# Optimization experiments

Measured on AMD Instinct MI355X. Metric: run time of the kernel, lower is better.

## Reference

```python
import jax, jax.numpy as jnp
import numpy as np

D_MODEL = 256
D_INNER = 512   # expand=2
D_STATE = 16
DT_RANK = 16    # ceil(d_model/16)
D_CONV = 4
N_LAYERS = 2    # per direction
B, N = 2, 1024


def _mamba_layer(x, W_in, cw, cb, W_x, W_dt, b_dt, A_log, Dp, W_out):
    """One mamba_ssm.Mamba forward. x: (B, L, d_model)."""
    Bb, L, _ = x.shape
    xz = x @ W_in.T                        # (B, L, 2*d_inner)
    di = xz.shape[-1] // 2
    xc, z = xz[..., :di], xz[..., di:]
    # causal depthwise conv1d, kernel D_CONV, left-pad d_conv-1
    K = cw.shape[-1]
    xp = jnp.pad(xc, ((0, 0), (K - 1, 0), (0, 0)))
    xc = sum(xp[:, k:k + L, :] * cw[:, k] for k in range(K)) + cb
    xc = jax.nn.silu(xc)
    # input-dependent dt, B, C
    dbl = xc @ W_x.T                       # (B, L, dt_rank + 2*d_state)
    ds = A_log.shape[-1]
    dt = dbl[..., :DT_RANK]
    Bm = dbl[..., DT_RANK:DT_RANK + ds]    # (B, L, d_state)
    Cm = dbl[..., DT_RANK + ds:]           # (B, L, d_state)
    dt = jax.nn.softplus(dt @ W_dt.T + b_dt)  # (B, L, d_inner)
    A = -jnp.exp(A_log)                    # (d_inner, d_state)
    dA = jnp.exp(dt[..., None] * A)                          # (B, L, di, ds)
    dBx = dt[..., None] * Bm[:, :, None, :] * xc[..., None]  # (B, L, di, ds)

    def step(h, inp):
        a_t, b_t, c_t = inp                # (B,di,ds),(B,di,ds),(B,ds)
        h = a_t * h + b_t
        y_t = jnp.einsum('bds,bs->bd', h, c_t)
        return h, y_t

    h0 = jnp.zeros((Bb, di, ds), x.dtype)
    _, ys = jax.lax.scan(step, h0, (dA.transpose(1, 0, 2, 3),
                                    dBx.transpose(1, 0, 2, 3),
                                    Cm.transpose(1, 0, 2)))
    y = ys.transpose(1, 0, 2) + xc * Dp    # skip term D*x
    y = y * jax.nn.silu(z)                 # gate
    return y @ W_out.T                     # (B, L, d_model)


def setup_inputs() -> dict:
    key = jax.random.key(0)
    ks = jax.random.split(key, 10)
    s = 0.05  # weight scale for numerical stability
    nlay = 2 * N_LAYERS  # forward layers then backward layers
    return {
        "x": jax.random.normal(ks[0], (B, N, D_MODEL), jnp.float32),
        "in_proj": jax.random.normal(ks[1], (nlay, 2 * D_INNER, D_MODEL), jnp.float32) * s,
        "conv_w": jax.random.normal(ks[2], (nlay, D_INNER, D_CONV), jnp.float32) * s,
        "conv_b": jax.random.normal(ks[3], (nlay, D_INNER), jnp.float32) * s,
        "x_proj": jax.random.normal(ks[4], (nlay, DT_RANK + 2 * D_STATE, D_INNER), jnp.float32) * s,
        "dt_proj": jax.random.normal(ks[5], (nlay, D_INNER, DT_RANK), jnp.float32) * s,
        "dt_bias": jax.random.normal(ks[6], (nlay, D_INNER), jnp.float32) * s,
        "A_log": jax.random.uniform(ks[7], (nlay, D_INNER, D_STATE), jnp.float32),
        "D": jax.random.uniform(ks[8], (nlay, D_INNER), jnp.float32),
        "out_proj": jax.random.normal(ks[9], (nlay, D_MODEL, D_INNER), jnp.float32) * s,
    }


def reference(x, in_proj, conv_w, conv_b, x_proj, dt_proj, dt_bias, A_log, D, out_proj):
    n = in_proj.shape[0] // 2
    x_fwd = x
    for i in range(n):
        x_fwd = _mamba_layer(x_fwd, in_proj[i], conv_w[i], conv_b[i], x_proj[i],
                             dt_proj[i], dt_bias[i], A_log[i], D[i], out_proj[i])
    x_bwd = x[:, ::-1, :]
    for i in range(n, 2 * n):
        x_bwd = _mamba_layer(x_bwd, in_proj[i], conv_w[i], conv_b[i], x_proj[i],
                             dt_proj[i], dt_bias[i], A_log[i], D[i], out_proj[i])
    x_bwd = x_bwd[:, ::-1, :]
    return jnp.concatenate([x_fwd, x_bwd], axis=-1)  # (B, N, 2*d_model)
```

## Files before the change

### kernel.cpp

```cpp
#include <hip/hip_runtime.h>
#include <math.h>

#define G 2
#define BB 2
#define L 1024
#define DM 256
#define DI 512
#define DS 16
#define DR 16
#define CH 64
#define CL 16
#define RTOT (G*BB*L)
#define SKX 8
#define YSTR 520

#define NWIN  (4 * 2 * DI * DM)
#define NWOUT (4 * DM * DI)

typedef short bh8 __attribute__((ext_vector_type(8)));
typedef float f4x __attribute__((ext_vector_type(4)));

__device__ __forceinline__ float silu_f(float x) { return x / (1.f + __expf(-x)); }
__device__ __forceinline__ float softplus_f(float x) {
    return (x > 20.f) ? x : __logf(1.f + __expf(x));
}

__device__ __forceinline__ unsigned short f2bf(float f) {
    unsigned u = __float_as_uint(f);
    unsigned r = u + 0x7FFFu + ((u >> 16) & 1u);
    return (unsigned short)(r >> 16);
}
__device__ __forceinline__ float bf2f(unsigned short s) {
    return __uint_as_float(((unsigned)s) << 16);
}

__global__ __launch_bounds__(256) void cvtW2(
    const float* __restrict__ Wa, short* __restrict__ Wah, short* __restrict__ Wal, int n4a,
    const float* __restrict__ Wb, short* __restrict__ Wbh, short* __restrict__ Wbl, int n4b)
{
    int i = blockIdx.x * 256 + threadIdx.x;
    const float* W; short *Wh, *Wl;
    if (i < n4a) { W = Wa; Wh = Wah; Wl = Wal; }
    else if (i < n4a + n4b) { i -= n4a; W = Wb; Wh = Wbh; Wl = Wbl; }
    else return;
    float4 v = *(const float4*)&W[(size_t)i * 4];
    short4 h, l;
    unsigned short s;
    s = f2bf(v.x); h.x = (short)s; l.x = (short)f2bf(v.x - bf2f(s));
    s = f2bf(v.y); h.y = (short)s; l.y = (short)f2bf(v.y - bf2f(s));
    s = f2bf(v.z); h.z = (short)s; l.z = (short)f2bf(v.z - bf2f(s));
    s = f2bf(v.w); h.w = (short)s; l.w = (short)f2bf(v.w - bf2f(s));
    *(short4*)&Wh[(size_t)i * 4] = h;
    *(short4*)&Wl[(size_t)i * 4] = l;
}

template<int AMAP>
__global__ __launch_bounds__(256) void mfma_inproj(
    const float* __restrict__ Ax,
    const short* __restrict__ Ah, const short* __restrict__ Al,
    const short* __restrict__ Wh, const short* __restrict__ Wl,
    int step, float* __restrict__ C)
{
    constexpr int BM = 128, Ktot = DM, Nout = 2 * DI, ldc = 1024;
    __shared__ short As_hi[BM * 40];
    __shared__ short As_lo[BM * 40];
    __shared__ short Bs_hi[64 * 40];
    __shared__ short Bs_lo[64 * 40];

    const int row0 = blockIdx.y * BM;
    const int col0 = blockIdx.x * 64;
    const int g    = row0 >> 11;
    const int lay  = g * 2 + step;
    const short* Whg = Wh + (size_t)lay * Nout * Ktot;
    const short* Wlg = Wl + (size_t)lay * Nout * Ktot;
    const int t    = threadIdx.x;
    const int lane = t & 63, wv = t >> 6;
    const int m = lane & 15, quad = lane >> 4;
    const int wr = wv >> 1, wc = wv & 1;
    const int NT = Ktot / 32;

    float4 pa[4];
    short4 pah[4], pal[4], pbh[2], pbl[2];
    auto loadT = [&](int kt) {
        const int kb = kt * 32;
        #pragma unroll
        for (int i = 0; i < 4; i++) {
            int id = t + 256 * i;
            int row = id >> 3, kq = id & 7;
            if (AMAP == 1) {
                int gr = row0 + row;
                int gg = gr >> 11, b = (gr >> 10) & 1, l = gr & 1023;
                int sl = gg ? (1023 - l) : l;
                pa[i] = *(const float4*)&Ax[(size_t)(b * 1024 + sl) * Ktot + kb + kq * 4];
            } else {
                size_t o = (size_t)(row0 + row) * Ktot + kb + kq * 4;
                pah[i] = *(const short4*)&Ah[o];
                pal[i] = *(const short4*)&Al[o];
            }
        }
        #pragma unroll
        for (int i = 0; i < 2; i++) {
            int id = t + 256 * i;
            int row = id >> 3, kq = id & 7;
            size_t o = (size_t)(col0 + row) * Ktot + kb + kq * 4;
            pbh[i] = *(const short4*)&Whg[o];
            pbl[i] = *(const short4*)&Wlg[o];
        }
    };

    f4x acc[4][2] = {};
    loadT(0);

    for (int kt = 0; kt < NT; kt++) {
        #pragma unroll
        for (int i = 0; i < 4; i++) {
            int id = t + 256 * i;
            int row = id >> 3, kq = id & 7;
            if (AMAP == 1) {
                float4 v = pa[i];
                short4 h, l;
                unsigned short s;
                s = f2bf(v.x); h.x = (short)s; l.x = (short)f2bf(v.x - bf2f(s));
                s = f2bf(v.y); h.y = (short)s; l.y = (short)f2bf(v.y - bf2f(s));
                s = f2bf(v.z); h.z = (short)s; l.z = (short)f2bf(v.z - bf2f(s));
                s = f2bf(v.w); h.w = (short)s; l.w = (short)f2bf(v.w - bf2f(s));
                *(short4*)&As_hi[row * 40 + kq * 4] = h;
                *(short4*)&As_lo[row * 40 + kq * 4] = l;
            } else {
                *(short4*)&As_hi[row * 40 + kq * 4] = pah[i];
                *(short4*)&As_lo[row * 40 + kq * 4] = pal[i];
            }
        }
        #pragma unroll
        for (int i = 0; i < 2; i++) {
            int id = t + 256 * i;
            int row = id >> 3, kq = id & 7;
            *(short4*)&Bs_hi[row * 40 + kq * 4] = pbh[i];
            *(short4*)&Bs_lo[row * 40 + kq * 4] = pbl[i];
        }
        __syncthreads();
        if (kt + 1 < NT) loadT(kt + 1);

        bh8 ah[4], al[4], bh[2], bl[2];
        #pragma unroll
        for (int p = 0; p < 4; p++) {
            int r = wr * 64 + p * 16 + m;
            ah[p] = *(bh8*)&As_hi[r * 40 + quad * 8];
            al[p] = *(bh8*)&As_lo[r * 40 + quad * 8];
        }
        #pragma unroll
        for (int q = 0; q < 2; q++) {
            int r = wc * 32 + q * 16 + m;
            bh[q] = *(bh8*)&Bs_hi[r * 40 + quad * 8];
            bl[q] = *(bh8*)&Bs_lo[r * 40 + quad * 8];
        }
        #pragma unroll
        for (int p = 0; p < 4; p++)
            #pragma unroll
            for (int q = 0; q < 2; q++) {
                acc[p][q] = __builtin_amdgcn_mfma_f32_16x16x32_bf16(ah[p], bh[q], acc[p][q], 0, 0, 0);
                acc[p][q] = __builtin_amdgcn_mfma_f32_16x16x32_bf16(ah[p], bl[q], acc[p][q], 0, 0, 0);
                acc[p][q] = __builtin_amdgcn_mfma_f32_16x16x32_bf16(al[p], bh[q], acc[p][q], 0, 0, 0);
            }
        __syncthreads();
    }

    #pragma unroll
    for (int p = 0; p < 4; p++)
        #pragma unroll
        for (int q = 0; q < 2; q++) {
            int gcol = col0 + wc * 32 + q * 16 + m;
            #pragma unroll
            for (int r = 0; r < 4; r++) {
                int grow = row0 + wr * 64 + p * 16 + quad * 4 + r;
                C[(size_t)grow * ldc + gcol] = acc[p][q][r];
            }
        }
}

template<int SPLITK>
__global__ __launch_bounds__(256) void gemm_xproj(
    const float* __restrict__ XZ, const float* __restrict__ cw,
    const float* __restrict__ cb, float* __restrict__ XCb,
    const float* __restrict__ W, int step,
    float* __restrict__ C, size_t partStride)
{
    constexpr int Nout = 48, Ktot = DI;
    __shared__ float As[16][68];
    __shared__ float Bs[16][68];

    const int row0 = blockIdx.y * 64;
    const int g    = row0 >> 11;
    const int lay  = g * 2 + step;
    const float* Wg = W + (size_t)lay * Nout * Ktot;
    const int t  = threadIdx.x;
    const int tx = t & 15, ty = t >> 4;
    const int Kc    = Ktot / SPLITK;
    const int kbase = blockIdx.z * Kc;
    const int NT    = Kc / 16;

    const int sr = t >> 2;
    const int sk = (t & 3) * 4;
    const int gr = row0 + sr;
    const int l  = gr & 1023;
    const bool bok = (sr < Nout);

    float4 pa, pb;
    auto loadT = [&](int kt) {
        const int ch = kbase + kt * 16 + sk;
        const float* wb = cw + ((size_t)lay * 512 + ch) * 4;
        float4 w0 = *(const float4*)&wb[0];
        float4 w1 = *(const float4*)&wb[4];
        float4 w2 = *(const float4*)&wb[8];
        float4 w3 = *(const float4*)&wb[12];
        float4 acc = *(const float4*)&cb[(size_t)lay * 512 + ch];
        #pragma unroll
        for (int k = 0; k < 4; k++) {
            if (l - 3 + k < 0) continue;
            float4 xv = *(const float4*)&XZ[(size_t)(gr - 3 + k) * 1024 + ch];
            acc.x += (&w0.x)[k] * xv.x; acc.y += (&w1.x)[k] * xv.y;
            acc.z += (&w2.x)[k] * xv.z; acc.w += (&w3.x)[k] * xv.w;
        }
        acc.x = silu_f(acc.x); acc.y = silu_f(acc.y);
        acc.z = silu_f(acc.z); acc.w = silu_f(acc.w);
        pa = acc;
        *(float4*)&XCb[(size_t)gr * 512 + ch] = acc;
        pb = bok ? *(const float4*)&Wg[(size_t)sr * Ktot + kbase + kt * 16 + sk]
                 : make_float4(0.f, 0.f, 0.f, 0.f);
    };

    float acc[4][4] = {};
    loadT(0);

    for (int kt = 0; kt < NT; kt++) {
        As[sk + 0][sr] = pa.x; As[sk + 1][sr] = pa.y;
        As[sk + 2][sr] = pa.z; As[sk + 3][sr] = pa.w;
        Bs[sk + 0][sr] = pb.x; Bs[sk + 1][sr] = pb.y;
        Bs[sk + 2][sr] = pb.z; Bs[sk + 3][sr] = pb.w;
        __syncthreads();
        if (kt + 1 < NT) loadT(kt + 1);
        #pragma unroll
        for (int kk = 0; kk < 16; kk++) {
            float4 a = *(const float4*)&As[kk][ty * 4];
            float4 b = *(const float4*)&Bs[kk][tx * 4];
            float av[4] = {a.x, a.y, a.z, a.w};
            float bv[4] = {b.x, b.y, b.z, b.w};
            #pragma unroll
            for (int i = 0; i < 4; i++)
                #pragma unroll
                for (int j = 0; j < 4; j++) acc[i][j] += av[i] * bv[j];
        }
        __syncthreads();
    }

    float* Cz = C + (size_t)blockIdx.z * partStride;
    const int col = tx * 4;
    if (col < Nout) {
        #pragma unroll
        for (int i = 0; i < 4; i++) {
            int r = row0 + ty * 4 + i;
            *(float4*)&Cz[(size_t)r * 48 + col] =
                make_float4(acc[i][0], acc[i][1], acc[i][2], acc[i][3]);
        }
    }
}

__global__ __launch_bounds__(512) void scanA(
    const float* __restrict__ XCb, const float* __restrict__ Pdbl,
    const float* __restrict__ A_log, const float* __restrict__ Wdt,
    const float* __restrict__ bdt, float* __restrict__ DBLc,
    float* __restrict__ Aprod, float* __restrict__ Hend, int step)
{
    __shared__ float dbl[CL][48];
    int blk = blockIdx.x;
    int c  = blk & (CH - 1);
    int gb = blk >> 6;
    int g  = gb >> 1;
    int lay = g * 2 + step;
    int d = threadIdx.x;
    int r0 = gb * L + c * CL;

    for (int id = threadIdx.x; id < CL * 48; id += 512) {
        int rr = id / 48, cc = id - rr * 48;
        size_t o = (size_t)(r0 + rr) * 48 + cc;
        float v = 0.f;
        #pragma unroll
        for (int s = 0; s < SKX; s++) v += Pdbl[(size_t)s * (RTOT * 48) + o];
        dbl[rr][cc] = v;
        DBLc[o] = v;
    }

    float wdt[16];
    const float* wrow = Wdt + ((size_t)lay * DI + d) * DR;
    #pragma unroll
    for (int k = 0; k < 16; k += 4) {
        float4 v = *(const float4*)&wrow[k];
        wdt[k] = v.x; wdt[k + 1] = v.y; wdt[k + 2] = v.z; wdt[k + 3] = v.w;
    }
    float bias = bdt[(size_t)lay * DI + d];

    float a[DS], h[DS], ap[DS];
    const float* al = A_log + ((size_t)lay * DI + d) * DS;
    #pragma unroll
    for (int s = 0; s < DS; s++) { a[s] = -__expf(al[s]); h[s] = 0.f; ap[s] = 1.f; }
    float xc_next = XCb[(size_t)r0 * DI + d];
    __syncthreads();

    for (int tt = 0; tt < CL; tt++) {
        float xcv = xc_next;
        if (tt + 1 < CL) xc_next = XCb[(size_t)(r0 + tt + 1) * DI + d];
        float dtr = bias;
        #pragma unroll
        for (int k = 0; k < 16; k++) dtr += dbl[tt][k] * wdt[k];
        float dt = softplus_f(dtr);
        float dx = dt * xcv;
        #pragma unroll
        for (int s = 0; s < DS; s++) {
            float da = __expf(dt * a[s]);
            h[s] = da * h[s] + dx * dbl[tt][16 + s];
            ap[s] *= da;
        }
    }
    size_t base = ((size_t)(gb * DI + d) * CH + c) * DS;
    #pragma unroll
    for (int q = 0; q < 4; q++) {
        *(float4*)&Aprod[base + q * 4] = make_float4(ap[q*4], ap[q*4+1], ap[q*4+2], ap[q*4+3]);
        *(float4*)&Hend [base + q * 4] = make_float4(h[q*4],  h[q*4+1],  h[q*4+2],  h[q*4+3]);
    }
}

__global__ __launch_bounds__(256) void scanCombine(
    const float* __restrict__ Aprod, const float* __restrict__ Hend,
    float* __restrict__ Hinit)
{
    int idx = blockIdx.x * 256 + threadIdx.x;
    int s  = idx & 15;
    int gd = idx >> 4;
    size_t base = (size_t)gd * CH * DS + s;
    float h = 0.f;
    for (int c0 = 0; c0 < CH; c0 += 8) {
        float ap[8], e[8];
        #pragma unroll
        for (int j = 0; j < 8; j++) {
            size_t o = base + (size_t)(c0 + j) * DS;
            ap[j] = Aprod[o]; e[j] = Hend[o];
        }
        #pragma unroll
        for (int j = 0; j < 8; j++) {
            Hinit[base + (size_t)(c0 + j) * DS] = h;
            h = ap[j] * h + e[j];
        }
    }
}

template<int OUTMODE>
__global__ __launch_bounds__(512) void scanB_fused(
    const float* __restrict__ XCb, const float* __restrict__ DBLc,
    const float* __restrict__ XZ, const float* __restrict__ A_log,
    const float* __restrict__ Wdt, const float* __restrict__ bdt,
    const float* __restrict__ Dp, const float* __restrict__ Hinit,
    const short* __restrict__ Woh, const short* __restrict__ Wol,
    float* __restrict__ Cout, short* __restrict__ Ph, short* __restrict__ Pl,
    int step)
{
    __shared__ float dbl[CL][48];
    __shared__ short Ys_hi[CL * YSTR];
    __shared__ short Ys_lo[CL * YSTR];
    int blk = blockIdx.x;
    int c  = blk & (CH - 1);
    int gb = blk >> 6;
    int g  = gb >> 1;
    int lay = g * 2 + step;
    int d = threadIdx.x;
    int r0 = gb * L + c * CL;

    for (int id = threadIdx.x; id < CL * 48; id += 512) {
        int rr = id / 48, cc = id - rr * 48;
        dbl[rr][cc] = DBLc[(size_t)(r0 + rr) * 48 + cc];
    }

    float xc[CL], zz[CL];
    #pragma unroll
    for (int tt = 0; tt < CL; tt++) xc[tt] = XCb[(size_t)(r0 + tt) * DI + d];
    #pragma unroll
    for (int tt = 0; tt < CL; tt++) zz[tt] = XZ[(size_t)(r0 + tt) * 1024 + 512 + d];

    float wdt[16];
    const float* wrow = Wdt + ((size_t)lay * DI + d) * DR;
    #pragma unroll
    for (int k = 0; k < 16; k += 4) {
        float4 v = *(const float4*)&wrow[k];
        wdt[k] = v.x; wdt[k + 1] = v.y; wdt[k + 2] = v.z; wdt[k + 3] = v.w;
    }
    float bias = bdt[(size_t)lay * DI + d];

    float a[DS], h[DS];
    const float* al = A_log + ((size_t)lay * DI + d) * DS;
    size_t base = ((size_t)(gb * DI + d) * CH + c) * DS;
    #pragma unroll
    for (int q = 0; q < 4; q++) {
        float4 hv = *(const float4*)&Hinit[base + q * 4];
        h[q*4] = hv.x; h[q*4+1] = hv.y; h[q*4+2] = hv.z; h[q*4+3] = hv.w;
    }
    #pragma unroll
    for (int s = 0; s < DS; s++) a[s] = -__expf(al[s]);
    float Dv = Dp[(size_t)lay * DI + d];
    __syncthreads();

    #pragma unroll
    for (int tt = 0; tt < CL; tt++) {
        float dtr = bias;
        #pragma unroll
        for (int k = 0; k < 16; k++) dtr += dbl[tt][k] * wdt[k];
        float dt = softplus_f(dtr);
        float dx = dt * xc[tt];
        float y = 0.f;
        #pragma unroll
        for (int s = 0; s < DS; s++) {
            float da = __expf(dt * a[s]);
            h[s] = da * h[s] + dx * dbl[tt][16 + s];
            y += h[s] * dbl[tt][32 + s];
        }
        y += xc[tt] * Dv;
        y *= silu_f(zz[tt]);
        unsigned short hs = f2bf(y);
        Ys_hi[tt * YSTR + d] = (short)hs;
        Ys_lo[tt * YSTR + d] = (short)f2bf(y - bf2f(hs));
    }
    __syncthreads();

    const int lane = threadIdx.x & 63, wv = threadIdx.x >> 6;
    const int m = lane & 15, quad = lane >> 4;
    const size_t wbase = (size_t)lay * DM * DI;

    #pragma unroll
    for (int q = 0; q < 2; q++) {
        const int coln = wv * 32 + q * 16 + m;
        const size_t wrow2 = wbase + (size_t)coln * DI;
        bh8 wh[16], wl[16];
        #pragma unroll
        for (int i = 0; i < 16; i++) {
            const int kk = i * 32 + quad * 8;
            wh[i] = *(const bh8*)&Woh[wrow2 + kk];
            wl[i] = *(const bh8*)&Wol[wrow2 + kk];
        }
        f4x acc = {};
        #pragma unroll
        for (int i = 0; i < 16; i++) {
            const int kk = i * 32 + quad * 8;
            bh8 ahv = *(bh8*)&Ys_hi[m * YSTR + kk];
            bh8 alv = *(bh8*)&Ys_lo[m * YSTR + kk];
            acc = __builtin_amdgcn_mfma_f32_16x16x32_bf16(ahv, wh[i], acc, 0, 0, 0);
            acc = __builtin_amdgcn_mfma_f32_16x16x32_bf16(ahv, wl[i], acc, 0, 0, 0);
            acc = __builtin_amdgcn_mfma_f32_16x16x32_bf16(alv, wh[i], acc, 0, 0, 0);
        }
        #pragma unroll
        for (int r = 0; r < 4; r++) {
            int tt = quad * 4 + r;
            int grow = r0 + tt;
            if (OUTMODE == 0) {
                size_t o = (size_t)grow * DM + coln;
                unsigned short hs = f2bf(acc[r]);
                Ph[o] = (short)hs;
                Pl[o] = (short)f2bf(acc[r] - bf2f(hs));
            } else {
                int b = (grow >> 10) & 1, l = grow & 1023;
                size_t dst = (g == 0)
                    ? ((size_t)(b * 1024 + l) * 512 + coln)
                    : ((size_t)(b * 1024 + (1023 - l)) * 512 + 256 + coln);
                Cout[dst] = acc[r];
            }
        }
    }
}

extern "C" void kernel_launch(void* const* d_in, const int* in_sizes, int n_in,
                              void* d_out, int out_size, void* d_ws, size_t ws_size,
                              hipStream_t stream)
{
    const float* x        = (const float*)d_in[0];
    const float* in_proj  = (const float*)d_in[1];
    const float* conv_w   = (const float*)d_in[2];
    const float* conv_b   = (const float*)d_in[3];
    const float* x_proj   = (const float*)d_in[4];
    const float* dt_proj  = (const float*)d_in[5];
    const float* dt_bias  = (const float*)d_in[6];
    const float* A_log    = (const float*)d_in[7];
    const float* Dp       = (const float*)d_in[8];
    const float* out_proj = (const float*)d_in[9];
    float* out = (float*)d_out;

    float* w = (float*)d_ws;
    size_t o = 0;
    float* XZ    = w + o; o += (size_t)RTOT * 1024;
    float* XCb   = w + o; o += (size_t)RTOT * DI;
    float* Pdbl  = w + o; o += (size_t)SKX * RTOT * 48;
    float* DBLc  = w + o; o += (size_t)RTOT * 48;
    float* Aprod = w + o; o += (size_t)G * BB * DI * CH * DS;
    float* Hend  = w + o; o += (size_t)G * BB * DI * CH * DS;
    float* Hinit = w + o; o += (size_t)G * BB * DI * CH * DS;
    short* Wih   = (short*)(w + o); o += NWIN / 2;
    short* Wil   = (short*)(w + o); o += NWIN / 2;
    short* Woh   = (short*)(w + o); o += NWOUT / 2;
    short* Wol   = (short*)(w + o); o += NWOUT / 2;
    short* Ph    = (short*)(w + o); o += (size_t)RTOT * DM / 2;
    short* Pl    = (short*)(w + o); o += (size_t)RTOT * DM / 2;
    (void)ws_size; (void)in_sizes; (void)n_in; (void)out_size;

    {
        int n4a = NWIN / 4, n4b = NWOUT / 4;
        cvtW2<<<(n4a + n4b + 255) / 256, 256, 0, stream>>>(
            in_proj, Wih, Wil, n4a, out_proj, Woh, Wol, n4b);
    }

    for (int step = 0; step < 2; step++) {
        if (step == 0)
            mfma_inproj<1><<<dim3(16, 32), 256, 0, stream>>>(
                x, nullptr, nullptr, Wih, Wil, 0, XZ);
        else
            mfma_inproj<0><<<dim3(16, 32), 256, 0, stream>>>(
                nullptr, Ph, Pl, Wih, Wil, 1, XZ);

        gemm_xproj<SKX><<<dim3(1, 64, SKX), 256, 0, stream>>>(
            XZ, conv_w, conv_b, XCb, x_proj, step, Pdbl, (size_t)RTOT * 48);

        scanA<<<G * BB * CH, 512, 0, stream>>>(
            XCb, Pdbl, A_log, dt_proj, dt_bias, DBLc, Aprod, Hend, step);
        scanCombine<<<(G * BB * DI * DS) / 256, 256, 0, stream>>>(Aprod, Hend, Hinit);
        if (step == 0)
            scanB_fused<0><<<G * BB * CH, 512, 0, stream>>>(
                XCb, DBLc, XZ, A_log, dt_proj, dt_bias, Dp, Hinit,
                Woh, Wol, nullptr, Ph, Pl, 0);
        else
            scanB_fused<1><<<G * BB * CH, 512, 0, stream>>>(
                XCb, DBLc, XZ, A_log, dt_proj, dt_bias, Dp, Hinit,
                Woh, Wol, out, nullptr, nullptr, 1);
    }
}
```

Measured before the change: 241.6 us.

## Fuse all Mamba layer stages into one cooperative persistent kernel with grid syncs

Replaces the sequence of about a dozen kernel launches (weight conversion, in-projection, conv+x-projection, chunk scan, combine, output scan) with a single cooperative kernel of 256 blocks by 512 threads. The stages run in order inside it, separated by grid.sync(). Each block runs two 256-thread virtual tiles for the GEMM phases, and shared memory is a union across phases. This is meant to remove launch gaps and inter-kernel drain. The cost is that every grid-wide barrier waits for the slowest block, occupancy is fixed at one 512-thread block per CU, and the scan phases use fewer threads per block. If the cooperative launch fails, it falls back to the old multi-kernel path.

```diff
diff --git a/kernel.cpp b/kernel.cpp
--- a/kernel.cpp
+++ b/kernel.cpp
@@ -1,5 +1,8 @@
 #include <hip/hip_runtime.h>
+#include <hip/hip_cooperative_groups.h>
 #include <math.h>
+
+namespace cg = cooperative_groups;
 
 #define G 2
 #define BB 2
@@ -13,6 +16,8 @@
 #define RTOT (G*BB*L)
 #define SKX 8
 #define YSTR 520
+#define NBLK 256
+#define NTHR 512
 
 #define NWIN  (4 * 2 * DI * DM)
 #define NWOUT (4 * DM * DI)
@@ -34,46 +39,50 @@
     return __uint_as_float(((unsigned)s) << 16);
 }
 
-__global__ __launch_bounds__(256) void cvtW2(
-    const float* __restrict__ Wa, short* __restrict__ Wah, short* __restrict__ Wal, int n4a,
-    const float* __restrict__ Wb, short* __restrict__ Wbh, short* __restrict__ Wbl, int n4b)
-{
-    int i = blockIdx.x * 256 + threadIdx.x;
-    const float* W; short *Wh, *Wl;
-    if (i < n4a) { W = Wa; Wh = Wah; Wl = Wal; }
-    else if (i < n4a + n4b) { i -= n4a; W = Wb; Wh = Wbh; Wl = Wbl; }
-    else return;
-    float4 v = *(const float4*)&W[(size_t)i * 4];
-    short4 h, l;
-    unsigned short s;
-    s = f2bf(v.x); h.x = (short)s; l.x = (short)f2bf(v.x - bf2f(s));
-    s = f2bf(v.y); h.y = (short)s; l.y = (short)f2bf(v.y - bf2f(s));
-    s = f2bf(v.z); h.z = (short)s; l.z = (short)f2bf(v.z - bf2f(s));
-    s = f2bf(v.w); h.w = (short)s; l.w = (short)f2bf(v.w - bf2f(s));
-    *(short4*)&Wh[(size_t)i * 4] = h;
-    *(short4*)&Wl[(size_t)i * 4] = l;
-}
+struct SmemIP {
+    short As_hi[2][128 * 40];
+    short As_lo[2][128 * 40];
+    short Bs_hi[2][64 * 40];
+    short Bs_lo[2][64 * 40];
+};
+struct SmemXP {
+    float As[2][16][68];
+    float Bs[2][16][68];
+};
+struct SmemSC {
+    float dbl[CL][48];
+    float xcs[CL][DI];
+    float dts[CL][DI];
+    short Ys_hi[CL * YSTR];
+    short Ys_lo[CL * YSTR];
+};
+union Smem {
+    SmemIP ip;
+    SmemXP xp;
+    SmemSC sc;
+};
 
 template<int AMAP>
-__global__ __launch_bounds__(256) void mfma_inproj(
+__device__ __forceinline__ void ip_phase(
     const float* __restrict__ Ax,
     const short* __restrict__ Ah, const short* __restrict__ Al,
     const short* __restrict__ Wh, const short* __restrict__ Wl,
-    int step, float* __restrict__ C)
-{
-    constexpr int BM = 128, Ktot = DM, Nout = 2 * DI, ldc = 1024;
-    __shared__ short As_hi[BM * 40];
-    __shared__ short As_lo[BM * 40];
-    __shared__ short Bs_hi[64 * 40];
-    __shared__ short Bs_lo[64 * 40];
-
-    const int row0 = blockIdx.y * BM;
-    const int col0 = blockIdx.x * 64;
+    int step, float* __restrict__ C, Smem& sm, int blk, int tid)
+{
+    constexpr int Ktot = DM, Nout = 2 * DI, ldc = 1024;
+    const int half = tid >> 8;
+    const int t    = tid & 255;
+    const int vb   = blk * 2 + half;
+    const int row0 = (vb >> 4) * 128;
+    const int col0 = (vb & 15) * 64;
     const int g    = row0 >> 11;
     const int lay  = g * 2 + step;
     const short* Whg = Wh + (size_t)lay * Nout * Ktot;
     const short* Wlg = Wl + (size_t)lay * Nout * Ktot;
-    const int t    = threadIdx.x;
+    short* As_hi = sm.ip.As_hi[half];
+    short* As_lo = sm.ip.As_lo[half];
+    short* Bs_hi = sm.ip.Bs_hi[half];
+    short* Bs_lo = sm.ip.Bs_lo[half];
     const int lane = t & 63, wv = t >> 6;
     const int m = lane & 15, quad = lane >> 4;
     const int wr = wv >> 1, wc = wv & 1;
@@ -178,6 +187,483 @@
         }
 }
 
+__device__ __forceinline__ void xp_phase(
+    const float* __restrict__ XZ, const float* __restrict__ cw,
+    const float* __restrict__ cb, float* __restrict__ XCb,
+    const float* __restrict__ W, int step,
+    float* __restrict__ Cc, size_t partStride, Smem& sm, int blk, int tid)
+{
+    constexpr int Nout = 48, Ktot = DI;
+    const int half = tid >> 8;
+    const int t    = tid & 255;
+    const int vb   = blk * 2 + half;
+    const int by   = vb & 63, bz = vb >> 6;
+    float (*As)[68] = sm.xp.As[half];
+    float (*Bs)[68] = sm.xp.Bs[half];
+
+    const int row0 = by * 64;
+    const int g    = row0 >> 11;
+    const int lay  = g * 2 + step;
+    const float* Wg = W + (size_t)lay * Nout * Ktot;
+    const int tx = t & 15, ty = t >> 4;
+    const int Kc    = Ktot / SKX;
+    const int kbase = bz * Kc;
+    const int NT    = Kc / 16;
+
+    const int sr = t >> 2;
+    const int sk = (t & 3) * 4;
+    const int gr = row0 + sr;
+    const int l  = gr & 1023;
+    const bool bok = (sr < Nout);
+
+    float4 pa, pb;
+    auto loadT = [&](int kt) {
+        const int ch = kbase + kt * 16 + sk;
+        const float* wb = cw + ((size_t)lay * 512 + ch) * 4;
+        float4 w0 = *(const float4*)&wb[0];
+        float4 w1 = *(const float4*)&wb[4];
+        float4 w2 = *(const float4*)&wb[8];
+        float4 w3 = *(const float4*)&wb[12];
+        float4 acc = *(const float4*)&cb[(size_t)lay * 512 + ch];
+        #pragma unroll
+        for (int k = 0; k < 4; k++) {
+            if (l - 3 + k < 0) continue;
+            float4 xv = *(const float4*)&XZ[(size_t)(gr - 3 + k) * 1024 + ch];
+            acc.x += (&w0.x)[k] * xv.x; acc.y += (&w1.x)[k] * xv.y;
+            acc.z += (&w2.x)[k] * xv.z; acc.w += (&w3.x)[k] * xv.w;
+        }
+        acc.x = silu_f(acc.x); acc.y = silu_f(acc.y);
+        acc.z = silu_f(acc.z); acc.w = silu_f(acc.w);
+        pa = acc;
+        *(float4*)&XCb[(size_t)gr * 512 + ch] = acc;
+        pb = bok ? *(const float4*)&Wg[(size_t)sr * Ktot + kbase + kt * 16 + sk]
+                 : make_float4(0.f, 0.f, 0.f, 0.f);
+    };
+
+    float acc[4][4] = {};
+    loadT(0);
+
+    for (int kt = 0; kt < NT; kt++) {
+        As[sk + 0][sr] = pa.x; As[sk + 1][sr] = pa.y;
+        As[sk + 2][sr] = pa.z; As[sk + 3][sr] = pa.w;
+        Bs[sk + 0][sr] = pb.x; Bs[sk + 1][sr] = pb.y;
+        Bs[sk + 2][sr] = pb.z; Bs[sk + 3][sr] = pb.w;
+        __syncthreads();
+        if (kt + 1 < NT) loadT(kt + 1);
+        #pragma unroll
+        for (int kk = 0; kk < 16; kk++) {
+            float4 a = *(const float4*)&As[kk][ty * 4];
+            float4 b = *(const float4*)&Bs[kk][tx * 4];
+            float av[4] = {a.x, a.y, a.z, a.w};
+            float bv[4] = {b.x, b.y, b.z, b.w};
+            #pragma unroll
+            for (int i = 0; i < 4; i++)
+                #pragma unroll
+                for (int j = 0; j < 4; j++) acc[i][j] += av[i] * bv[j];
+        }
+        __syncthreads();
+    }
+
+    float* Cz = Cc + (size_t)bz * partStride;
+    const int col = tx * 4;
+    if (col < Nout) {
+        #pragma unroll
+        for (int i = 0; i < 4; i++) {
+            int r = row0 + ty * 4 + i;
+            *(float4*)&Cz[(size_t)r * 48 + col] =
+                make_float4(acc[i][0], acc[i][1], acc[i][2], acc[i][3]);
+        }
+    }
+}
+
+__device__ __forceinline__ void sa_phase(
+    const float* __restrict__ XCb, const float* __restrict__ Pdbl,
+    const float* __restrict__ A_log, const float* __restrict__ Wdt,
+    const float* __restrict__ bdt,
+    float* __restrict__ Aprod, float* __restrict__ Hend, int step,
+    Smem& sm, int blk, int tid)
+{
+    const int c  = blk & (CH - 1);
+    const int gb = blk >> 6;
+    const int g  = gb >> 1;
+    const int lay = g * 2 + step;
+    const int d  = tid;
+    const int r0 = gb * L + c * CL;
+
+    for (int id = tid; id < CL * 48; id += NTHR) {
+        int rr = id / 48, cc = id - rr * 48;
+        size_t o = (size_t)(r0 + rr) * 48 + cc;
+        float v = 0.f;
+        #pragma unroll
+        for (int s = 0; s < SKX; s++) v += Pdbl[(size_t)s * (RTOT * 48) + o];
+        sm.sc.dbl[rr][cc] = v;
+    }
+    #pragma unroll
+    for (int tt = 0; tt < CL; tt++)
+        sm.sc.xcs[tt][d] = XCb[(size_t)(r0 + tt) * DI + d];
+
+    float wdt[16];
+    const float* wrow = Wdt + ((size_t)lay * DI + d) * DR;
+    #pragma unroll
+    for (int k = 0; k < 16; k += 4) {
+        float4 v = *(const float4*)&wrow[k];
+        wdt[k] = v.x; wdt[k + 1] = v.y; wdt[k + 2] = v.z; wdt[k + 3] = v.w;
+    }
+    float bias = bdt[(size_t)lay * DI + d];
+
+    float a[DS], h[DS], ap[DS];
+    const float* al = A_log + ((size_t)lay * DI + d) * DS;
+    #pragma unroll
+    for (int s = 0; s < DS; s++) { a[s] = -__expf(al[s]); h[s] = 0.f; ap[s] = 1.f; }
+    __syncthreads();
+
+    for (int tt = 0; tt < CL; tt++) {
+        float dtr = bias;
+        #pragma unroll
+        for (int k = 0; k < 16; k++) dtr += sm.sc.dbl[tt][k] * wdt[k];
+        float dt = softplus_f(dtr);
+        sm.sc.dts[tt][d] = dt;
+        float dx = dt * sm.sc.xcs[tt][d];
+        #pragma unroll
+        for (int s = 0; s < DS; s++) {
+            float da = __expf(dt * a[s]);
+            h[s] = da * h[s] + dx * sm.sc.dbl[tt][16 + s];
+            ap[s] *= da;
+        }
+    }
+    size_t base = ((size_t)(gb * DI + d) * CH + c) * DS;
+    #pragma unroll
+    for (int q = 0; q < 4; q++) {
+        *(float4*)&Aprod[base + q * 4] = make_float4(ap[q*4], ap[q*4+1], ap[q*4+2], ap[q*4+3]);
+        *(float4*)&Hend [base + q * 4] = make_float4(h[q*4],  h[q*4+1],  h[q*4+2],  h[q*4+3]);
+    }
+}
+
+__device__ __forceinline__ void comb_phase(
+    const float* __restrict__ Aprod, const float* __restrict__ Hend,
+    float* __restrict__ Hinit, int gid)
+{
+    if (gid < G * BB * DI * DS) {
+        int s  = gid & 15;
+        int gd = gid >> 4;
+        size_t base = (size_t)gd * CH * DS + s;
+        float h = 0.f;
+        for (int c0 = 0; c0 < CH; c0 += 8) {
+            float ap[8], e[8];
+            #pragma unroll
+            for (int j = 0; j < 8; j++) {
+                size_t o = base + (size_t)(c0 + j) * DS;
+                ap[j] = Aprod[o]; e[j] = Hend[o];
+            }
+            #pragma unroll
+            for (int j = 0; j < 8; j++) {
+                Hinit[base + (size_t)(c0 + j) * DS] = h;
+                h = ap[j] * h + e[j];
+            }
+        }
+    }
+}
+
+template<int OUTMODE>
+__device__ __forceinline__ void sb_phase(
+    const float* __restrict__ XZ, const float* __restrict__ A_log,
+    const float* __restrict__ Dp, const float* __restrict__ Hinit,
+    const short* __restrict__ Woh, const short* __restrict__ Wol,
+    float* __restrict__ Cout, short* __restrict__ Ph, short* __restrict__ Pl,
+    int step, Smem& sm, int blk, int tid)
+{
+    const int c  = blk & (CH - 1);
+    const int gb = blk >> 6;
+    const int g  = gb >> 1;
+    const int lay = g * 2 + step;
+    const int d  = tid;
+    const int r0 = gb * L + c * CL;
+
+    float zz[CL];
+    #pragma unroll
+    for (int tt = 0; tt < CL; tt++) zz[tt] = XZ[(size_t)(r0 + tt) * 1024 + 512 + d];
+
+    float a[DS], h[DS];
+    const float* al = A_log + ((size_t)lay * DI + d) * DS;
+    size_t base = ((size_t)(gb * DI + d) * CH + c) * DS;
+    #pragma unroll
+    for (int q = 0; q < 4; q++) {
+        float4 hv = *(const float4*)&Hinit[base + q * 4];
+        h[q*4] = hv.x; h[q*4+1] = hv.y; h[q*4+2] = hv.z; h[q*4+3] = hv.w;
+    }
+    #pragma unroll
+    for (int s = 0; s < DS; s++) a[s] = -__expf(al[s]);
+    float Dv = Dp[(size_t)lay * DI + d];
+
+    #pragma unroll
+    for (int tt = 0; tt < CL; tt++) {
+        float dt  = sm.sc.dts[tt][d];
+        float xcv = sm.sc.xcs[tt][d];
+        float dx = dt * xcv;
+        float y = 0.f;
+        #pragma unroll
+        for (int s = 0; s < DS; s++) {
+            float da = __expf(dt * a[s]);
+            h[s] = da * h[s] + dx * sm.sc.dbl[tt][16 + s];
+            y += h[s] * sm.sc.dbl[tt][32 + s];
+        }
+        y += xcv * Dv;
+        y *= silu_f(zz[tt]);
+        unsigned short hs = f2bf(y);
+        sm.sc.Ys_hi[tt * YSTR + d] = (short)hs;
+        sm.sc.Ys_lo[tt * YSTR + d] = (short)f2bf(y - bf2f(hs));
+    }
+    __syncthreads();
+
+    const int lane = tid & 63, wv = tid >> 6;
+    const int m = lane & 15, quad = lane >> 4;
+    const size_t wbase = (size_t)lay * DM * DI;
+
+    #pragma unroll
+    for (int q = 0; q < 2; q++) {
+        const int coln = wv * 32 + q * 16 + m;
+        const size_t wrow2 = wbase + (size_t)coln * DI;
+        bh8 wh[16], wl[16];
+        #pragma unroll
+        for (int i = 0; i < 16; i++) {
+            const int kk = i * 32 + quad * 8;
+            wh[i] = *(const bh8*)&Woh[wrow2 + kk];
+            wl[i] = *(const bh8*)&Wol[wrow2 + kk];
+        }
+        f4x acc = {};
+        #pragma unroll
+        for (int i = 0; i < 16; i++) {
+            const int kk = i * 32 + quad * 8;
+            bh8 ahv = *(bh8*)&sm.sc.Ys_hi[m * YSTR + kk];
+            bh8 alv = *(bh8*)&sm.sc.Ys_lo[m * YSTR + kk];
+            acc = __builtin_amdgcn_mfma_f32_16x16x32_bf16(ahv, wh[i], acc, 0, 0, 0);
+            acc = __builtin_amdgcn_mfma_f32_16x16x32_bf16(ahv, wl[i], acc, 0, 0, 0);
+            acc = __builtin_amdgcn_mfma_f32_16x16x32_bf16(alv, wh[i], acc, 0, 0, 0);
+        }
+        #pragma unroll
+        for (int r = 0; r < 4; r++) {
+            int tt = quad * 4 + r;
+            int grow = r0 + tt;
+            if (OUTMODE == 0) {
+                size_t o = (size_t)grow * DM + coln;
+                unsigned short hs = f2bf(acc[r]);
+                Ph[o] = (short)hs;
+                Pl[o] = (short)f2bf(acc[r] - bf2f(hs));
+            } else {
+                int b = (grow >> 10) & 1, l = grow & 1023;
+                size_t dst = (g == 0)
+                    ? ((size_t)(b * 1024 + l) * 512 + coln)
+                    : ((size_t)(b * 1024 + (1023 - l)) * 512 + 256 + coln);
+                Cout[dst] = acc[r];
+            }
+        }
+    }
+}
+
+__global__ __launch_bounds__(NTHR) void mamba_mega(
+    const float* __restrict__ x, const float* __restrict__ in_proj,
+    const float* __restrict__ conv_w, const float* __restrict__ conv_b,
+    const float* __restrict__ x_proj, const float* __restrict__ dt_proj,
+    const float* __restrict__ dt_bias, const float* __restrict__ A_log,
+    const float* __restrict__ Dp, const float* __restrict__ out_proj,
+    float* __restrict__ out,
+    float* __restrict__ XZ, float* __restrict__ XCb, float* __restrict__ Pdbl,
+    float* __restrict__ Aprod, float* __restrict__ Hend, float* __restrict__ Hinit,
+    short* __restrict__ Wih, short* __restrict__ Wil,
+    short* __restrict__ Woh, short* __restrict__ Wol,
+    short* __restrict__ Ph, short* __restrict__ Pl)
+{
+    cg::grid_group grid = cg::this_grid();
+    __shared__ Smem sm;
+    const int blk = blockIdx.x;
+    const int tid = threadIdx.x;
+    const int gid = blk * NTHR + tid;
+
+    {
+        constexpr int n4a = NWIN / 4, n4b = NWOUT / 4;
+        for (int i = gid; i < n4a + n4b; i += NBLK * NTHR) {
+            int j = i; const float* Wsrc; short *Wh, *Wl;
+            if (j < n4a) { Wsrc = in_proj; Wh = Wih; Wl = Wil; }
+            else { j -= n4a; Wsrc = out_proj; Wh = Woh; Wl = Wol; }
+            float4 v = *(const float4*)&Wsrc[(size_t)j * 4];
+            short4 hh, ll;
+            unsigned short s;
+            s = f2bf(v.x); hh.x = (short)s; ll.x = (short)f2bf(v.x - bf2f(s));
+            s = f2bf(v.y); hh.y = (short)s; ll.y = (short)f2bf(v.y - bf2f(s));
+            s = f2bf(v.z); hh.z = (short)s; ll.z = (short)f2bf(v.z - bf2f(s));
+            s = f2bf(v.w); hh.w = (short)s; ll.w = (short)f2bf(v.w - bf2f(s));
+            *(short4*)&Wh[(size_t)j * 4] = hh;
+            *(short4*)&Wl[(size_t)j * 4] = ll;
+        }
+    }
+    grid.sync();
+
+    ip_phase<1>(x, nullptr, nullptr, Wih, Wil, 0, XZ, sm, blk, tid);
+    grid.sync();
+    xp_phase(XZ, conv_w, conv_b, XCb, x_proj, 0, Pdbl, (size_t)RTOT * 48, sm, blk, tid);
+    grid.sync();
+    sa_phase(XCb, Pdbl, A_log, dt_proj, dt_bias, Aprod, Hend, 0, sm, blk, tid);
+    grid.sync();
+    comb_phase(Aprod, Hend, Hinit, gid);
+    grid.sync();
+    sb_phase<0>(XZ, A_log, Dp, Hinit, Woh, Wol, nullptr, Ph, Pl, 0, sm, blk, tid);
+    grid.sync();
+
+    ip_phase<0>(nullptr, Ph, Pl, Wih, Wil, 1, XZ, sm, blk, tid);
+    grid.sync();
+    xp_phase(XZ, conv_w, conv_b, XCb, x_proj, 1, Pdbl, (size_t)RTOT * 48, sm, blk, tid);
+    grid.sync();
+    sa_phase(XCb, Pdbl, A_log, dt_proj, dt_bias, Aprod, Hend, 1, sm, blk, tid);
+    grid.sync();
+    comb_phase(Aprod, Hend, Hinit, gid);
+    grid.sync();
+    sb_phase<1>(XZ, A_log, Dp, Hinit, Woh, Wol, out, nullptr, nullptr, 1, sm, blk, tid);
+}
+
+__global__ __launch_bounds__(256) void cvtW2(
+    const float* __restrict__ Wa, short* __restrict__ Wah, short* __restrict__ Wal, int n4a,
+    const float* __restrict__ Wb, short* __restrict__ Wbh, short* __restrict__ Wbl, int n4b)
+{
+    int i = blockIdx.x * 256 + threadIdx.x;
+    const float* W; short *Wh, *Wl;
+    if (i < n4a) { W = Wa; Wh = Wah; Wl = Wal; }
+    else if (i < n4a + n4b) { i -= n4a; W = Wb; Wh = Wbh; Wl = Wbl; }
+    else return;
+    float4 v = *(const float4*)&W[(size_t)i * 4];
+    short4 h, l;
+    unsigned short s;
+    s = f2bf(v.x); h.x = (short)s; l.x = (short)f2bf(v.x - bf2f(s));
+    s = f2bf(v.y); h.y = (short)s; l.y = (short)f2bf(v.y - bf2f(s));
+    s = f2bf(v.z); h.z = (short)s; l.z = (short)f2bf(v.z - bf2f(s));
+    s = f2bf(v.w); h.w = (short)s; l.w = (short)f2bf(v.w - bf2f(s));
+    *(short4*)&Wh[(size_t)i * 4] = h;
+    *(short4*)&Wl[(size_t)i * 4] = l;
+}
+
+template<int AMAP>
+__global__ __launch_bounds__(256) void mfma_inproj(
+    const float* __restrict__ Ax,
+    const short* __restrict__ Ah, const short* __restrict__ Al,
+    const short* __restrict__ Wh, const short* __restrict__ Wl,
+    int step, float* __restrict__ C)
+{
+    constexpr int BM = 128, Ktot = DM, Nout = 2 * DI, ldc = 1024;
+    __shared__ short As_hi[BM * 40];
+    __shared__ short As_lo[BM * 40];
+    __shared__ short Bs_hi[64 * 40];
+    __shared__ short Bs_lo[64 * 40];
+
+    const int row0 = blockIdx.y * BM;
+    const int col0 = blockIdx.x * 64;
+    const int g    = row0 >> 11;
+    const int lay  = g * 2 + step;
+    const short* Whg = Wh + (size_t)lay * Nout * Ktot;
+    const short* Wlg = Wl + (size_t)lay * Nout * Ktot;
+    const int t    = threadIdx.x;
+    const int lane = t & 63, wv = t >> 6;
+    const int m = lane & 15, quad = lane >> 4;
+    const int wr = wv >> 1, wc = wv & 1;
+    const int NT = Ktot / 32;
+
+    float4 pa[4];
+    short4 pah[4], pal[4], pbh[2], pbl[2];
+    auto loadT = [&](int kt) {
+        const int kb = kt * 32;
+        #pragma unroll
+        for (int i = 0; i < 4; i++) {
+            int id = t + 256 * i;
+            int row = id >> 3, kq = id & 7;
+            if (AMAP == 1) {
+                int gr = row0 + row;
+                int gg = gr >> 11, b = (gr >> 10) & 1, l = gr & 1023;
+                int sl = gg ? (1023 - l) : l;
+                pa[i] = *(const float4*)&Ax[(size_t)(b * 1024 + sl) * Ktot + kb + kq * 4];
+            } else {
+                size_t o = (size_t)(row0 + row) * Ktot + kb + kq * 4;
+                pah[i] = *(const short4*)&Ah[o];
+                pal[i] = *(const short4*)&Al[o];
+            }
+        }
+        #pragma unroll
+        for (int i = 0; i < 2; i++) {
+            int id = t + 256 * i;
+            int row = id >> 3, kq = id & 7;
+            size_t o = (size_t)(col0 + row) * Ktot + kb + kq * 4;
+            pbh[i] = *(const short4*)&Whg[o];
+            pbl[i] = *(const short4*)&Wlg[o];
+        }
+    };
+
+    f4x acc[4][2] = {};
+    loadT(0);
+
+    for (int kt = 0; kt < NT; kt++) {
+        #pragma unroll
+        for (int i = 0; i < 4; i++) {
+            int id = t + 256 * i;
+            int row = id >> 3, kq = id & 7;
+            if (AMAP == 1) {
+                float4 v = pa[i];
+                short4 h, l;
+                unsigned short s;
+                s = f2bf(v.x); h.x = (short)s; l.x = (short)f2bf(v.x - bf2f(s));
+                s = f2bf(v.y); h.y = (short)s; l.y = (short)f2bf(v.y - bf2f(s));
+                s = f2bf(v.z); h.z = (short)s; l.z = (short)f2bf(v.z - bf2f(s));
+                s = f2bf(v.w); h.w = (short)s; l.w = (short)f2bf(v.w - bf2f(s));
+                *(short4*)&As_hi[row * 40 + kq * 4] = h;
+                *(short4*)&As_lo[row * 40 + kq * 4] = l;
+            } else {
+                *(short4*)&As_hi[row * 40 + kq * 4] = pah[i];
+                *(short4*)&As_lo[row * 40 + kq * 4] = pal[i];
+            }
+        }
+        #pragma unroll
+        for (int i = 0; i < 2; i++) {
+            int id = t + 256 * i;
+            int row = id >> 3, kq = id & 7;
+            *(short4*)&Bs_hi[row * 40 + kq * 4] = pbh[i];
+            *(short4*)&Bs_lo[row * 40 + kq * 4] = pbl[i];
+        }
+        __syncthreads();
+        if (kt + 1 < NT) loadT(kt + 1);
+
+        bh8 ah[4], al[4], bh[2], bl[2];
+        #pragma unroll
+        for (int p = 0; p < 4; p++) {
+            int r = wr * 64 + p * 16 + m;
+            ah[p] = *(bh8*)&As_hi[r * 40 + quad * 8];
+            al[p] = *(bh8*)&As_lo[r * 40 + quad * 8];
+        }
+        #pragma unroll
+        for (int q = 0; q < 2; q++) {
+            int r = wc * 32 + q * 16 + m;
+            bh[q] = *(bh8*)&Bs_hi[r * 40 + quad * 8];
+            bl[q] = *(bh8*)&Bs_lo[r * 40 + quad * 8];
+        }
+        #pragma unroll
+        for (int p = 0; p < 4; p++)
+            #pragma unroll
+            for (int q = 0; q < 2; q++) {
+                acc[p][q] = __builtin_amdgcn_mfma_f32_16x16x32_bf16(ah[p], bh[q], acc[p][q], 0, 0, 0);
+                acc[p][q] = __builtin_amdgcn_mfma_f32_16x16x32_bf16(ah[p], bl[q], acc[p][q], 0, 0, 0);
+                acc[p][q] = __builtin_amdgcn_mfma_f32_16x16x32_bf16(al[p], bh[q], acc[p][q], 0, 0, 0);
+            }
+        __syncthreads();
+    }
+
+    #pragma unroll
+    for (int p = 0; p < 4; p++)
+        #pragma unroll
+        for (int q = 0; q < 2; q++) {
+            int gcol = col0 + wc * 32 + q * 16 + m;
+            #pragma unroll
+            for (int r = 0; r < 4; r++) {
+                int grow = row0 + wr * 64 + p * 16 + quad * 4 + r;
+                C[(size_t)grow * ldc + gcol] = acc[p][q][r];
+            }
+        }
+}
+
 template<int SPLITK>
 __global__ __launch_bounds__(256) void gemm_xproj(
     const float* __restrict__ XZ, const float* __restrict__ cw,
@@ -507,12 +993,25 @@
     short* Pl    = (short*)(w + o); o += (size_t)RTOT * DM / 2;
     (void)ws_size; (void)in_sizes; (void)n_in; (void)out_size;
 
+    void* kargs[] = {
+        (void*)&x, (void*)&in_proj, (void*)&conv_w, (void*)&conv_b,
+        (void*)&x_proj, (void*)&dt_proj, (void*)&dt_bias, (void*)&A_log,
+        (void*)&Dp, (void*)&out_proj, (void*)&out,
+        (void*)&XZ, (void*)&XCb, (void*)&Pdbl,
+        (void*)&Aprod, (void*)&Hend, (void*)&Hinit,
+        (void*)&Wih, (void*)&Wil, (void*)&Woh, (void*)&Wol,
+        (void*)&Ph, (void*)&Pl };
+    hipError_t err = hipLaunchCooperativeKernel(
+        reinterpret_cast<void*>(mamba_mega), dim3(NBLK), dim3(NTHR),
+        kargs, 0, stream);
+    if (err == hipSuccess) return;
+    (void)hipGetLastError();
+
     {
         int n4a = NWIN / 4, n4b = NWOUT / 4;
         cvtW2<<<(n4a + n4b + 255) / 256, 256, 0, stream>>>(
             in_proj, Wih, Wil, n4a, out_proj, Woh, Wol, n4b);
     }
-
     for (int step = 0; step < 2; step++) {
         if (step == 0)
             mfma_inproj<1><<<dim3(16, 32), 256, 0, stream>>>(
```

After: 598.2 us. +147.6%, slower.

## Fuse conv and x_proj GEMM into chunk scan kernel using split-bf16 MFMA

Applied to the files above, without the earlier changes.

Removes the separate split-K fp32 x_proj GEMM kernel and folds the causal conv, SiLU and x_proj projection into the first scan pass. Each chunk block computes its 16 rows of xc in registers, stores hi/lo bf16 parts to shared memory, and runs three-term bf16 MFMAs against pre-split x_proj weights, reducing per-wave partials in LDS. This cuts one launch per step, the partial-sum buffer round trip and the reload of xc. In exchange the scan kernel uses more LDS and registers, and the GEMM runs on only 256 blocks with small tiles.

```diff
diff --git a/kernel.cpp b/kernel.cpp
--- a/kernel.cpp
+++ b/kernel.cpp
@@ -11,11 +11,12 @@
 #define CH 64
 #define CL 16
 #define RTOT (G*BB*L)
-#define SKX 8
 #define YSTR 520
+#define XSTR 520
 
 #define NWIN  (4 * 2 * DI * DM)
 #define NWOUT (4 * DM * DI)
+#define NWX   (4 * 48 * DI)
 
 typedef short bh8 __attribute__((ext_vector_type(8)));
 typedef float f4x __attribute__((ext_vector_type(4)));
@@ -34,14 +35,16 @@
     return __uint_as_float(((unsigned)s) << 16);
 }
 
-__global__ __launch_bounds__(256) void cvtW2(
+__global__ __launch_bounds__(256) void cvtW3(
     const float* __restrict__ Wa, short* __restrict__ Wah, short* __restrict__ Wal, int n4a,
-    const float* __restrict__ Wb, short* __restrict__ Wbh, short* __restrict__ Wbl, int n4b)
+    const float* __restrict__ Wb, short* __restrict__ Wbh, short* __restrict__ Wbl, int n4b,
+    const float* __restrict__ Wc, short* __restrict__ Wch, short* __restrict__ Wcl, int n4c)
 {
     int i = blockIdx.x * 256 + threadIdx.x;
     const float* W; short *Wh, *Wl;
     if (i < n4a) { W = Wa; Wh = Wah; Wl = Wal; }
     else if (i < n4a + n4b) { i -= n4a; W = Wb; Wh = Wbh; Wl = Wbl; }
+    else if (i < n4a + n4b + n4c) { i -= n4a + n4b; W = Wc; Wh = Wch; Wl = Wcl; }
     else return;
     float4 v = *(const float4*)&W[(size_t)i * 4];
     short4 h, l;
@@ -178,116 +181,85 @@
         }
 }
 
-template<int SPLITK>
-__global__ __launch_bounds__(256) void gemm_xproj(
+__global__ __launch_bounds__(512) void scanA2(
     const float* __restrict__ XZ, const float* __restrict__ cw,
-    const float* __restrict__ cb, float* __restrict__ XCb,
-    const float* __restrict__ W, int step,
-    float* __restrict__ C, size_t partStride)
-{
-    constexpr int Nout = 48, Ktot = DI;
-    __shared__ float As[16][68];
-    __shared__ float Bs[16][68];
-
-    const int row0 = blockIdx.y * 64;
-    const int g    = row0 >> 11;
-    const int lay  = g * 2 + step;
-    const float* Wg = W + (size_t)lay * Nout * Ktot;
-    const int t  = threadIdx.x;
-    const int tx = t & 15, ty = t >> 4;
-    const int Kc    = Ktot / SPLITK;
-    const int kbase = blockIdx.z * Kc;
-    const int NT    = Kc / 16;
-
-    const int sr = t >> 2;
-    const int sk = (t & 3) * 4;
-    const int gr = row0 + sr;
-    const int l  = gr & 1023;
-    const bool bok = (sr < Nout);
-
-    float4 pa, pb;
-    auto loadT = [&](int kt) {
-        const int ch = kbase + kt * 16 + sk;
-        const float* wb = cw + ((size_t)lay * 512 + ch) * 4;
-        float4 w0 = *(const float4*)&wb[0];
-        float4 w1 = *(const float4*)&wb[4];
-        float4 w2 = *(const float4*)&wb[8];
-        float4 w3 = *(const float4*)&wb[12];
-        float4 acc = *(const float4*)&cb[(size_t)lay * 512 + ch];
-        #pragma unroll
-        for (int k = 0; k < 4; k++) {
-            if (l - 3 + k < 0) continue;
-            float4 xv = *(const float4*)&XZ[(size_t)(gr - 3 + k) * 1024 + ch];
-            acc.x += (&w0.x)[k] * xv.x; acc.y += (&w1.x)[k] * xv.y;
-            acc.z += (&w2.x)[k] * xv.z; acc.w += (&w3.x)[k] * xv.w;
-        }
-        acc.x = silu_f(acc.x); acc.y = silu_f(acc.y);
-        acc.z = silu_f(acc.z); acc.w = silu_f(acc.w);
-        pa = acc;
-        *(float4*)&XCb[(size_t)gr * 512 + ch] = acc;
-        pb = bok ? *(const float4*)&Wg[(size_t)sr * Ktot + kbase + kt * 16 + sk]
-                 : make_float4(0.f, 0.f, 0.f, 0.f);
-    };
-
-    float acc[4][4] = {};
-    loadT(0);
-
-    for (int kt = 0; kt < NT; kt++) {
-        As[sk + 0][sr] = pa.x; As[sk + 1][sr] = pa.y;
-        As[sk + 2][sr] = pa.z; As[sk + 3][sr] = pa.w;
-        Bs[sk + 0][sr] = pb.x; Bs[sk + 1][sr] = pb.y;
-        Bs[sk + 2][sr] = pb.z; Bs[sk + 3][sr] = pb.w;
-        __syncthreads();
-        if (kt + 1 < NT) loadT(kt + 1);
-        #pragma unroll
-        for (int kk = 0; kk < 16; kk++) {
-            float4 a = *(const float4*)&As[kk][ty * 4];
-            float4 b = *(const float4*)&Bs[kk][tx * 4];
-            float av[4] = {a.x, a.y, a.z, a.w};
-            float bv[4] = {b.x, b.y, b.z, b.w};
-            #pragma unroll
-            for (int i = 0; i < 4; i++)
-                #pragma unroll
-                for (int j = 0; j < 4; j++) acc[i][j] += av[i] * bv[j];
-        }
-        __syncthreads();
-    }
-
-    float* Cz = C + (size_t)blockIdx.z * partStride;
-    const int col = tx * 4;
-    if (col < Nout) {
-        #pragma unroll
-        for (int i = 0; i < 4; i++) {
-            int r = row0 + ty * 4 + i;
-            *(float4*)&Cz[(size_t)r * 48 + col] =
-                make_float4(acc[i][0], acc[i][1], acc[i][2], acc[i][3]);
-        }
-    }
-}
-
-__global__ __launch_bounds__(512) void scanA(
-    const float* __restrict__ XCb, const float* __restrict__ Pdbl,
+    const float* __restrict__ cb,
+    const short* __restrict__ Wxh, const short* __restrict__ Wxl,
     const float* __restrict__ A_log, const float* __restrict__ Wdt,
-    const float* __restrict__ bdt, float* __restrict__ DBLc,
+    const float* __restrict__ bdt,
+    float* __restrict__ XCb, float* __restrict__ DBLc,
     float* __restrict__ Aprod, float* __restrict__ Hend, int step)
 {
+    __shared__ short xcH[CL * XSTR];
+    __shared__ short xcL[CL * XSTR];
+    __shared__ float part[8][CL][48];
     __shared__ float dbl[CL][48];
-    int blk = blockIdx.x;
-    int c  = blk & (CH - 1);
-    int gb = blk >> 6;
-    int g  = gb >> 1;
-    int lay = g * 2 + step;
-    int d = threadIdx.x;
-    int r0 = gb * L + c * CL;
-
-    for (int id = threadIdx.x; id < CL * 48; id += 512) {
-        int rr = id / 48, cc = id - rr * 48;
-        size_t o = (size_t)(r0 + rr) * 48 + cc;
+
+    const int blk = blockIdx.x;
+    const int c  = blk & (CH - 1);
+    const int gb = blk >> 6;
+    const int g  = gb >> 1;
+    const int lay = g * 2 + step;
+    const int d  = threadIdx.x;
+    const int r0 = gb * L + c * CL;
+
+    float4 w4 = *(const float4*)&cw[((size_t)lay * DI + d) * 4];
+    float cbv = cb[(size_t)lay * DI + d];
+    float xz[CL + 3];
+    #pragma unroll
+    for (int j = 0; j < CL + 3; j++) {
+        int lr = c * CL + j - 3;
+        xz[j] = (lr < 0) ? 0.f : XZ[(size_t)(gb * L + lr) * 1024 + d];
+    }
+    float xc[CL];
+    #pragma unroll
+    for (int tt = 0; tt < CL; tt++) {
+        float v = cbv + w4.x * xz[tt] + w4.y * xz[tt + 1]
+                      + w4.z * xz[tt + 2] + w4.w * xz[tt + 3];
+        v = silu_f(v);
+        xc[tt] = v;
+        XCb[(size_t)(r0 + tt) * DI + d] = v;
+        unsigned short hs = f2bf(v);
+        xcH[tt * XSTR + d] = (short)hs;
+        xcL[tt * XSTR + d] = (short)f2bf(v - bf2f(hs));
+    }
+    __syncthreads();
+
+    {
+        const int lane = d & 63, wv = d >> 6;
+        const int m = lane & 15, quad = lane >> 4;
+        const int ks = wv * 64;
+        const size_t wb = (size_t)lay * 48 * DI;
+        f4x acc[3] = {};
+        #pragma unroll
+        for (int kt = 0; kt < 2; kt++) {
+            const int kb = ks + kt * 32 + quad * 8;
+            bh8 ah = *(bh8*)&xcH[m * XSTR + kb];
+            bh8 al = *(bh8*)&xcL[m * XSTR + kb];
+            #pragma unroll
+            for (int f = 0; f < 3; f++) {
+                bh8 bh = *(const bh8*)&Wxh[wb + (size_t)(f * 16 + m) * DI + kb];
+                bh8 bl = *(const bh8*)&Wxl[wb + (size_t)(f * 16 + m) * DI + kb];
+                acc[f] = __builtin_amdgcn_mfma_f32_16x16x32_bf16(ah, bh, acc[f], 0, 0, 0);
+                acc[f] = __builtin_amdgcn_mfma_f32_16x16x32_bf16(ah, bl, acc[f], 0, 0, 0);
+                acc[f] = __builtin_amdgcn_mfma_f32_16x16x32_bf16(al, bh, acc[f], 0, 0, 0);
+            }
+        }
+        #pragma unroll
+        for (int f = 0; f < 3; f++)
+            #pragma unroll
+            for (int r = 0; r < 4; r++)
+                part[wv][quad * 4 + r][f * 16 + m] = acc[f][r];
+    }
+    __syncthreads();
+
+    for (int o = d; o < CL * 48; o += 512) {
+        int tt = o / 48, cc = o - tt * 48;
         float v = 0.f;
         #pragma unroll
-        for (int s = 0; s < SKX; s++) v += Pdbl[(size_t)s * (RTOT * 48) + o];
-        dbl[rr][cc] = v;
-        DBLc[o] = v;
+        for (int w = 0; w < 8; w++) v += part[w][tt][cc];
+        dbl[tt][cc] = v;
+        DBLc[(size_t)(r0 + tt) * 48 + cc] = v;
     }
 
     float wdt[16];
@@ -303,17 +275,14 @@
     const float* al = A_log + ((size_t)lay * DI + d) * DS;
     #pragma unroll
     for (int s = 0; s < DS; s++) { a[s] = -__expf(al[s]); h[s] = 0.f; ap[s] = 1.f; }
-    float xc_next = XCb[(size_t)r0 * DI + d];
     __syncthreads();
 
     for (int tt = 0; tt < CL; tt++) {
-        float xcv = xc_next;
-        if (tt + 1 < CL) xc_next = XCb[(size_t)(r0 + tt + 1) * DI + d];
         float dtr = bias;
         #pragma unroll
         for (int k = 0; k < 16; k++) dtr += dbl[tt][k] * wdt[k];
         float dt = softplus_f(dtr);
-        float dx = dt * xcv;
+        float dx = dt * xc[tt];
         #pragma unroll
         for (int s = 0; s < DS; s++) {
             float da = __expf(dt * a[s]);
@@ -494,7 +463,7 @@
     size_t o = 0;
     float* XZ    = w + o; o += (size_t)RTOT * 1024;
     float* XCb   = w + o; o += (size_t)RTOT * DI;
-    float* Pdbl  = w + o; o += (size_t)SKX * RTOT * 48;
+    float* Pdbl  = w + o; o += (size_t)8 * RTOT * 48;
     float* DBLc  = w + o; o += (size_t)RTOT * 48;
     float* Aprod = w + o; o += (size_t)G * BB * DI * CH * DS;
     float* Hend  = w + o; o += (size_t)G * BB * DI * CH * DS;
@@ -505,12 +474,15 @@
     short* Wol   = (short*)(w + o); o += NWOUT / 2;
     short* Ph    = (short*)(w + o); o += (size_t)RTOT * DM / 2;
     short* Pl    = (short*)(w + o); o += (size_t)RTOT * DM / 2;
+    short* Wxh   = (short*)Pdbl;
+    short* Wxl   = Wxh + NWX;
     (void)ws_size; (void)in_sizes; (void)n_in; (void)out_size;
 
     {
-        int n4a = NWIN / 4, n4b = NWOUT / 4;
-        cvtW2<<<(n4a + n4b + 255) / 256, 256, 0, stream>>>(
-            in_proj, Wih, Wil, n4a, out_proj, Woh, Wol, n4b);
+        int n4a = NWIN / 4, n4b = NWOUT / 4, n4c = NWX / 4;
+        cvtW3<<<(n4a + n4b + n4c + 255) / 256, 256, 0, stream>>>(
+            in_proj, Wih, Wil, n4a, out_proj, Woh, Wol, n4b,
+            x_proj, Wxh, Wxl, n4c);
     }
 
     for (int step = 0; step < 2; step++) {
@@ -521,12 +493,12 @@
             mfma_inproj<0><<<dim3(16, 32), 256, 0, stream>>>(
                 nullptr, Ph, Pl, Wih, Wil, 1, XZ);
 
-        gemm_xproj<SKX><<<dim3(1, 64, SKX), 256, 0, stream>>>(
-            XZ, conv_w, conv_b, XCb, x_proj, step, Pdbl, (size_t)RTOT * 48);
-
-        scanA<<<G * BB * CH, 512, 0, stream>>>(
-            XCb, Pdbl, A_log, dt_proj, dt_bias, DBLc, Aprod, Hend, step);
+        scanA2<<<G * BB * CH, 512, 0, stream>>>(
+            XZ, conv_w, conv_b, Wxh, Wxl, A_log, dt_proj, dt_bias,
+            XCb, DBLc, Aprod, Hend, step);
+
         scanCombine<<<(G * BB * DI * DS) / 256, 256, 0, stream>>>(Aprod, Hend, Hinit);
+
         if (step == 0)
             scanB_fused<0><<<G * BB * CH, 512, 0, stream>>>(
                 XCb, DBLc, XZ, A_log, dt_proj, dt_bias, Dp, Hinit,
```

Result: faster. 223.6 us (-7.5%).
